# Kernel tuning notes

Measured on AMD Instinct MI355X. Metric: run time of the kernel, lower is better.

## Reference

```python
import jax, jax.numpy as jnp
import numpy as np

ACOUSTIC_BOOKS = [1, 2, 3, 4, 5, 6, 7, 8, 9, 10, 11, 12, 13, 14, 15, 16, 17, 17, 17, 17, 17]


def setup_inputs() -> dict:
    key = jax.random.key(0)
    ks = jax.random.split(key, 6)
    B, C, T, D, K, NB = 4, 512, 4096, 256, 2048, 18
    return {
        "x": jax.random.normal(ks[0], (B, C, T), dtype=jnp.float32),
        "Win_s": jax.random.normal(ks[1], (D, C), dtype=jnp.float32) * 0.05,
        "Win_a": jax.random.normal(ks[2], (D, C), dtype=jnp.float32) * 0.05,
        "Wout_s": jax.random.normal(ks[3], (C, D), dtype=jnp.float32) * 0.05,
        "Wout_a": jax.random.normal(ks[4], (C, D), dtype=jnp.float32) * 0.05,
        "E": jax.random.normal(ks[5], (NB, K, D), dtype=jnp.float32),
    }


def _nearest(z, e):
    # z: [B, D, T], e: [K, D] -> codes [B, T] via argmin of squared euclidean dist
    zt = z.transpose(0, 2, 1)  # [B, T, D]
    d2 = (jnp.sum(zt * zt, axis=-1, keepdims=True)
          - 2.0 * jnp.einsum('btd,kd->btk', zt, e)
          + jnp.sum(e * e, axis=-1))  # [B, T, K]
    return jnp.argmin(d2, axis=-1)  # [B, T]


def reference(x, Win_s, Win_a, Wout_s, Wout_a, E):
    # ---- encode ----
    xs = jnp.einsum('dc,bct->bdt', Win_s, x)  # in_proj_s (1x1 conv, no bias)
    codes = [_nearest(xs, E[0])]
    xa = jnp.einsum('dc,bct->bdt', Win_a, x)  # in_proj_a
    for cb in ACOUSTIC_BOOKS:
        idx = _nearest(xa, E[cb])
        xa = xa - E[cb][idx].transpose(0, 2, 1)  # residual subtract (decode gather)
        codes.append(idx)
    codes = jnp.stack(codes, axis=1)  # [B, 22, T]

    # ---- decode ----
    semantic = E[0][codes[:, 0]].transpose(0, 2, 1)  # [B, D, T]
    acoustic = jnp.zeros_like(semantic)
    for i, cb in enumerate(ACOUSTIC_BOOKS):
        acoustic = acoustic + E[cb][codes[:, i + 1]].transpose(0, 2, 1)
    out = (jnp.einsum('cd,bdt->bct', Wout_s, semantic)
           + jnp.einsum('cd,bdt->bct', Wout_a, acoustic))  # [B, 512, T]
    return out, codes
```

## Files before the change

### kernel.cpp

```cpp
#include <hip/hip_runtime.h>
#include <float.h>

#define TT 4096
#define BB 4
#define CC 512
#define DD 256
#define KK 2048
#define MM (BB*TT)
#define NBOOKS 22
#define EPS_PAIR 0.3f
#define EPS_FULL 0.3f
#define ZSTR 260
#define RPB 32

typedef _Float16 half8_t __attribute__((ext_vector_type(8)));
typedef float f32x4 __attribute__((ext_vector_type(4)));

__device__ __forceinline__ void insert3(float& v1, int& i1, float& v2, int& i2,
                                        float& v3, float u, int c) {
  if (u < v1 || (u == v1 && c < i1)) {
    v3 = v2; v2 = v1; i2 = i1; v1 = u; i1 = c;
  } else if (u < v2 || (u == v2 && c < i2)) {
    v3 = v2; v2 = u; i2 = c;
  } else {
    v3 = fminf(v3, u);
  }
}

__device__ __forceinline__ void merge5(float& v1, int& i1, float& v2, int& i2,
                                       float& v3,
                                       float w1, int j1, float w2, int j2, float w3) {
  if (w1 < v1 || (w1 == v1 && j1 < i1)) {
    if (v1 < w2 || (v1 == w2 && i1 < j2)) {
      v3 = fminf(v2, w2);
      v2 = v1; i2 = i1;
    } else {
      v3 = fminf(v1, w3);
      v2 = w2; i2 = j2;
    }
    v1 = w1; i1 = j1;
  } else {
    if (w1 < v2 || (w1 == v2 && j1 < i2)) {
      v3 = fminf(v2, w2);
      v2 = w1; i2 = j1;
    } else {
      v3 = fminf(w1, v3);
    }
  }
}

__global__ __launch_bounds__(256) void proj_kernel(const float* __restrict__ x,
    const float* __restrict__ Ws, const float* __restrict__ Wa,
    float* __restrict__ xs, float* __restrict__ xa)
{
  __shared__ float xt[16*64];
  __shared__ float wsl[16*68];
  __shared__ float wal[16*68];
  const int tid = threadIdx.x;
  const int t0 = blockIdx.x*64, d0 = blockIdx.y*64, b = blockIdx.z;
  const int u = tid & 63, cq = tid >> 6;
  const int tx = tid & 15, ty = tid >> 4;
  const float* xb = x + (size_t)b*CC*TT;
  float accS[4][4] = {{0}}, accA[4][4] = {{0}};
  for (int c0 = 0; c0 < CC; c0 += 16) {
    __syncthreads();
    #pragma unroll
    for (int i = 0; i < 4; ++i) {
      int cc = cq*4 + i;
      xt[cc*64 + u] = xb[(size_t)(c0+cc)*TT + t0 + u];
    }
    {
      float4 wv = *(const float4*)&Ws[(size_t)(d0+u)*CC + c0 + cq*4];
      wsl[(cq*4+0)*68 + u] = wv.x; wsl[(cq*4+1)*68 + u] = wv.y;
      wsl[(cq*4+2)*68 + u] = wv.z; wsl[(cq*4+3)*68 + u] = wv.w;
      wv = *(const float4*)&Wa[(size_t)(d0+u)*CC + c0 + cq*4];
      wal[(cq*4+0)*68 + u] = wv.x; wal[(cq*4+1)*68 + u] = wv.y;
      wal[(cq*4+2)*68 + u] = wv.z; wal[(cq*4+3)*68 + u] = wv.w;
    }
    __syncthreads();
    #pragma unroll
    for (int cc = 0; cc < 16; ++cc) {
      float4 tq = *(const float4*)&xt[cc*64 + ty*4];
      float4 sq = *(const float4*)&wsl[cc*68 + tx*4];
      float4 aq = *(const float4*)&wal[cc*68 + tx*4];
      float tf[4] = {tq.x,tq.y,tq.z,tq.w};
      float sf[4] = {sq.x,sq.y,sq.z,sq.w};
      float af[4] = {aq.x,aq.y,aq.z,aq.w};
      #pragma unroll
      for (int i = 0; i < 4; ++i)
        #pragma unroll
        for (int j = 0; j < 4; ++j) {
          accS[i][j] = fmaf(tf[i], sf[j], accS[i][j]);
          accA[i][j] = fmaf(tf[i], af[j], accA[i][j]);
        }
    }
  }
  #pragma unroll
  for (int i = 0; i < 4; ++i) {
    size_t r = (size_t)b*TT + t0 + ty*4 + i;
    float4 o;
    o.x = accS[i][0]; o.y = accS[i][1]; o.z = accS[i][2]; o.w = accS[i][3];
    *(float4*)&xs[r*DD + d0 + tx*4] = o;
    o.x = accA[i][0]; o.y = accA[i][1]; o.z = accA[i][2]; o.w = accA[i][3];
    *(float4*)&xa[r*DD + d0 + tx*4] = o;
  }
}

__global__ __launch_bounds__(256) void e2_kernel(const float* __restrict__ E,
    float* __restrict__ e2)
{
  int gid = blockIdx.x*256 + threadIdx.x;
  int wid = gid >> 6, lane = gid & 63;
  if (wid < 18*KK) {
    float4 v = *(const float4*)&E[(size_t)wid*DD + lane*4];
    float s = v.x*v.x + v.y*v.y + v.z*v.z + v.w*v.w;
    #pragma unroll
    for (int m = 1; m <= 32; m <<= 1) s += __shfl_xor(s, m);
    if (lane == 0) e2[wid] = s;
  }
}

__global__ __launch_bounds__(256) void cvt_e16_kernel(const float* __restrict__ E,
    _Float16* __restrict__ E16)
{
  size_t i = ((size_t)blockIdx.x*256 + threadIdx.x)*8;
  float4 u = *(const float4*)&E[i];
  float4 v = *(const float4*)&E[i+4];
  half8_t h;
  h[0]=(_Float16)u.x; h[1]=(_Float16)u.y; h[2]=(_Float16)u.z; h[3]=(_Float16)u.w;
  h[4]=(_Float16)v.x; h[5]=(_Float16)v.y; h[6]=(_Float16)v.z; h[7]=(_Float16)v.w;
  *(half8_t*)&E16[i] = h;
}

__global__ __launch_bounds__(256) __attribute__((amdgpu_waves_per_eu(2)))
void fused_encode_kernel(
    const float* __restrict__ xs_g, const float* __restrict__ xa_g,
    const float* __restrict__ E, const _Float16* __restrict__ E16,
    const float* __restrict__ e2, int* __restrict__ codes0,
    float* __restrict__ codes_f, float* __restrict__ aco_g)
{
  const int tid = threadIdx.x;
  const int lane = tid & 63, wave = tid >> 6;
  const int ln15 = lane & 15, lq = lane >> 4;
  const int row0 = blockIdx.x * RPB;

  __shared__ float Z[RPB][ZSTR];
  __shared__ float L1v[4][RPB], L2v[4][RPB], L3v[4][RPB];
  __shared__ int   L1i[4][RPB], L2i[4][RPB];
  __shared__ int   codes_s[RPB];
  __shared__ int   flist[RPB], plist[RPB];
  __shared__ int   nfull, npair;
  __shared__ float zrow[DD];
  __shared__ double Rv[4];
  __shared__ int    Ri[4];

  const int ldr = tid & 31, cg = tid >> 5;
  const int sr = tid >> 3, sg = tid & 7;

  for (int ib = 0; ib < NBOOKS; ++ib) {
    const int book = (ib <= 17) ? ib : 17;
    const float*     Eb   = E   + (size_t)book*KK*DD;
    const _Float16*  E16b = E16 + (size_t)book*KK*DD;
    const float*     e2b  = e2  + (size_t)book*KK;

    if (ib <= 1) {
      const float* src = (ib == 0) ? xs_g : xa_g;
      const float* sp = src + (size_t)(row0 + ldr)*DD + cg*32;
      #pragma unroll
      for (int j = 0; j < 8; ++j)
        *(float4*)&Z[ldr][cg*32 + j*4] = *(const float4*)(sp + j*4);
    }
    if (tid == 0) { nfull = 0; npair = 0; }
    __syncthreads();

    half8_t A[2][8];
    #pragma unroll
    for (int mt = 0; mt < 2; ++mt) {
      #pragma unroll
      for (int ks = 0; ks < 8; ++ks) {
        const float* zp = &Z[mt*16 + ln15][lq*8 + ks*32];
        float4 u = *(const float4*)zp;
        float4 v = *(const float4*)(zp + 4);
        half8_t a;
        a[0]=(_Float16)u.x; a[1]=(_Float16)u.y; a[2]=(_Float16)u.z; a[3]=(_Float16)u.w;
        a[4]=(_Float16)v.x; a[5]=(_Float16)v.y; a[6]=(_Float16)v.z; a[7]=(_Float16)v.w;
        A[mt][ks] = a;
      }
    }

    float b1[2][4], b2[2][4], b3[2][4]; int i1[2][4], i2[2][4];
    #pragma unroll
    for (int mt = 0; mt < 2; ++mt)
      #pragma unroll
      for (int j = 0; j < 4; ++j) {
        b1[mt][j] = FLT_MAX; b2[mt][j] = FLT_MAX; b3[mt][j] = FLT_MAX;
        i1[mt][j] = 0x7fffffff; i2[mt][j] = 0x7fffffff;
      }

    const _Float16* ebase = E16b + (size_t)(wave*512 + ln15)*DD + lq*8;

    half8_t B[8], NB[4];
    #pragma unroll
    for (int ks = 0; ks < 8; ++ks) B[ks] = *(const half8_t*)(ebase + ks*32);

    for (int nt = 0; nt < 32; ++nt) {
      const _Float16* nx = ebase + (size_t)(nt+1)*16*DD;
      if (nt < 31) {
        NB[0] = *(const half8_t*)(nx + 0*32);
        NB[1] = *(const half8_t*)(nx + 1*32);
        NB[2] = *(const half8_t*)(nx + 2*32);
        NB[3] = *(const half8_t*)(nx + 3*32);
      }
      int code = wave*512 + nt*16 + ln15;
      float e2v = e2b[code];
      f32x4 acc[2];
      #pragma unroll
      for (int mt = 0; mt < 2; ++mt) acc[mt] = (f32x4){0.f,0.f,0.f,0.f};
      #pragma unroll
      for (int ks = 0; ks < 8; ++ks) {
        #pragma unroll
        for (int mt = 0; mt < 2; ++mt)
          acc[mt] = __builtin_amdgcn_mfma_f32_16x16x32_f16(A[mt][ks], B[ks], acc[mt], 0, 0, 0);
      }
      #pragma unroll
      for (int mt = 0; mt < 2; ++mt)
        #pragma unroll
        for (int j = 0; j < 4; ++j) {
          float u = fmaf(-2.f, acc[mt][j], e2v);
          insert3(b1[mt][j], i1[mt][j], b2[mt][j], i2[mt][j], b3[mt][j], u, code);
        }
      if (nt < 31) {
        B[0] = NB[0]; B[1] = NB[1]; B[2] = NB[2]; B[3] = NB[3];
        B[4] = *(const half8_t*)(nx + 4*32);
        B[5] = *(const half8_t*)(nx + 5*32);
        B[6] = *(const half8_t*)(nx + 6*32);
        B[7] = *(const half8_t*)(nx + 7*32);
      }
    }

    #pragma unroll
    for (int mt = 0; mt < 2; ++mt)
      #pragma unroll
      for (int j = 0; j < 4; ++j) {
        float v1 = b1[mt][j], v2 = b2[mt][j], v3 = b3[mt][j];
        int a1 = i1[mt][j], a2 = i2[mt][j];
        #pragma unroll
        for (int m = 1; m <= 8; m <<= 1) {
          float w1 = __shfl_xor(v1, m), w2 = __shfl_xor(v2, m), w3 = __shfl_xor(v3, m);
          int   j1 = __shfl_xor(a1, m), j2 = __shfl_xor(a2, m);
          merge5(v1, a1, v2, a2, v3, w1, j1, w2, j2, w3);
        }
        if (ln15 == 0) {
          int rl = mt*16 + lq*4 + j;
          L1v[wave][rl] = v1; L1i[wave][rl] = a1;
          L2v[wave][rl] = v2; L2i[wave][rl] = a2;
          L3v[wave][rl] = v3;
        }
      }
    __syncthreads();
    if (tid < RPB) {
      float v1 = L1v[0][tid], v2 = L2v[0][tid], v3 = L3v[0][tid];
      int a1 = L1i[0][tid], a2 = L2i[0][tid];
      #pragma unroll
      for (int w = 1; w < 4; ++w)
        merge5(v1, a1, v2, a2, v3,
               L1v[w][tid], L1i[w][tid], L2v[w][tid], L2i[w][tid], L3v[w][tid]);
      codes_s[tid] = a1;
      int rg = row0 + tid;
      codes_f[((size_t)(rg >> 12)*NBOOKS + ib)*TT + (rg & (TT-1))] = (float)a1;
      if (ib == 0) codes0[rg] = a1;
      if (v3 - v1 < EPS_FULL) {
        flist[atomicAdd(&nfull, 1)] = tid;
      } else if (v2 - v1 < EPS_PAIR) {
        plist[atomicAdd(&npair, 1)] = tid | (a1 << 6) | (a2 << 17);
      }
    }
    __syncthreads();

    int nfl = nfull;
    for (int f = 0; f < nfl; ++f) {
      int row = flist[f];
      if (tid < 64)
        *(float4*)&zrow[tid*4] = *(const float4*)&Z[row][tid*4];
      __syncthreads();
      double bestv = DBL_MAX; int besti = 0x7fffffff;
      #pragma unroll
      for (int q = 0; q < 8; ++q) {
        int k = q*256 + tid;
        const float* er = Eb + (size_t)k*DD;
        double s = 0.0;
        for (int d = 0; d < DD; d += 4) {
          float4 e = *(const float4*)(er + d);
          double d0 = (double)zrow[d+0] - (double)e.x; s += d0*d0;
          double d1 = (double)zrow[d+1] - (double)e.y; s += d1*d1;
          double d2 = (double)zrow[d+2] - (double)e.z; s += d2*d2;
          double d3 = (double)zrow[d+3] - (double)e.w; s += d3*d3;
        }
        if (s < bestv || (s == bestv && k < besti)) { bestv = s; besti = k; }
      }
      #pragma unroll
      for (int m = 1; m <= 32; m <<= 1) {
        double ov = __shfl_xor(bestv, m);
        int    oi = __shfl_xor(besti, m);
        if (ov < bestv || (ov == bestv && oi < besti)) { bestv = ov; besti = oi; }
      }
      if (lane == 0) { Rv[wave] = bestv; Ri[wave] = besti; }
      __syncthreads();
      if (tid == 0) {
        double bvv = Rv[0]; int bii = Ri[0];
        #pragma unroll
        for (int w = 1; w < 4; ++w)
          if (Rv[w] < bvv || (Rv[w] == bvv && Ri[w] < bii)) { bvv = Rv[w]; bii = Ri[w]; }
        codes_s[row] = bii;
        int rg = row0 + row;
        codes_f[((size_t)(rg >> 12)*NBOOKS + ib)*TT + (rg & (TT-1))] = (float)bii;
        if (ib == 0) codes0[rg] = bii;
      }
      __syncthreads();
    }

    {
      int npr = npair;
      for (int f = wave; f < npr; f += 4) {
        int pk = plist[f];
        int row = pk & 63;
        int c1 = (pk >> 6) & 2047, c2 = (pk >> 17) & 2047;
        int cc = (lane < 32) ? c1 : c2;
        const float* er = Eb + (size_t)cc*DD + (lane & 31)*8;
        const float* zr = &Z[row][(lane & 31)*8];
        double s = 0.0;
        #pragma unroll
        for (int d = 0; d < 8; ++d) {
          double df = (double)zr[d] - (double)er[d];
          s += df*df;
        }
        #pragma unroll
        for (int m = 1; m <= 16; m <<= 1) s += __shfl_xor(s, m);
        double so = __shfl_xor(s, 32);
        double d1 = (lane < 32) ? s : so;
        double d2 = (lane < 32) ? so : s;
        int win = (d2 < d1 || (d2 == d1 && c2 < c1)) ? c2 : c1;
        if (lane == 0) {
          codes_s[row] = win;
          int rg = row0 + row;
          codes_f[((size_t)(rg >> 12)*NBOOKS + ib)*TT + (rg & (TT-1))] = (float)win;
          if (ib == 0) codes0[rg] = win;
        }
      }
    }
    __syncthreads();

    if (ib >= 1) {
      int code = codes_s[sr];
      const float* er = Eb + (size_t)code*DD;
      #pragma unroll
      for (int j = 0; j < 8; ++j) {
        int c = sg*4 + j*32;
        float4 e = *(const float4*)(er + c);
        float4 z = *(const float4*)&Z[sr][c];
        z.x -= e.x; z.y -= e.y; z.z -= e.z; z.w -= e.w;
        *(float4*)&Z[sr][c] = z;
      }
    }
    __syncthreads();
  }

  {
    const float* xp = xa_g + (size_t)(row0 + ldr)*DD + cg*32;
    float*       ap = aco_g + (size_t)(row0 + ldr)*DD + cg*32;
    #pragma unroll
    for (int j = 0; j < 8; ++j) {
      float4 x0 = *(const float4*)(xp + j*4);
      float4 zf = *(const float4*)&Z[ldr][cg*32 + j*4];
      float4 o;
      o.x = x0.x - zf.x; o.y = x0.y - zf.y; o.z = x0.z - zf.z; o.w = x0.w - zf.w;
      *(float4*)(ap + j*4) = o;
    }
  }
}

__global__ __launch_bounds__(256) void final_kernel(
    const float* __restrict__ Wos, const float* __restrict__ Woa,
    const float* __restrict__ E0, const int* __restrict__ codes0,
    const float* __restrict__ aco, float* __restrict__ out)
{
  __shared__ float wsl[16*68], wal[16*68], sml[16*68], acl[16*68];
  const int tid = threadIdx.x;
  const int t0 = blockIdx.x*64, c0 = blockIdx.y*64, b = blockIdx.z;
  const int u = tid & 63, dq = tid >> 6;
  const int tx = tid & 15, ty = tid >> 4;
  int code = codes0[b*TT + t0 + u];
  const float* smr = E0 + (size_t)code*DD;
  const float* acr = aco + (size_t)(b*TT + t0 + u)*DD;
  const float* wsr = Wos + (size_t)(c0+u)*DD;
  const float* war = Woa + (size_t)(c0+u)*DD;
  float accS[4][4] = {{0}}, accA[4][4] = {{0}};
  for (int dc0 = 0; dc0 < DD; dc0 += 16) {
    __syncthreads();
    float4 v;
    v = *(const float4*)(wsr + dc0 + dq*4);
    wsl[(dq*4+0)*68+u]=v.x; wsl[(dq*4+1)*68+u]=v.y; wsl[(dq*4+2)*68+u]=v.z; wsl[(dq*4+3)*68+u]=v.w;
    v = *(const float4*)(war + dc0 + dq*4);
    wal[(dq*4+0)*68+u]=v.x; wal[(dq*4+1)*68+u]=v.y; wal[(dq*4+2)*68+u]=v.z; wal[(dq*4+3)*68+u]=v.w;
    v = *(const float4*)(smr + dc0 + dq*4);
    sml[(dq*4+0)*68+u]=v.x; sml[(dq*4+1)*68+u]=v.y; sml[(dq*4+2)*68+u]=v.z; sml[(dq*4+3)*68+u]=v.w;
    v = *(const float4*)(acr + dc0 + dq*4);
    acl[(dq*4+0)*68+u]=v.x; acl[(dq*4+1)*68+u]=v.y; acl[(dq*4+2)*68+u]=v.z; acl[(dq*4+3)*68+u]=v.w;
    __syncthreads();
    #pragma unroll
    for (int d = 0; d < 16; ++d) {
      float4 cs = *(const float4*)&wsl[d*68 + tx*4];
      float4 ca = *(const float4*)&wal[d*68 + tx*4];
      float4 ts = *(const float4*)&sml[d*68 + ty*4];
      float4 ta = *(const float4*)&acl[d*68 + ty*4];
      float csf[4]={cs.x,cs.y,cs.z,cs.w}, caf[4]={ca.x,ca.y,ca.z,ca.w};
      float tsf[4]={ts.x,ts.y,ts.z,ts.w}, taf[4]={ta.x,ta.y,ta.z,ta.w};
      #pragma unroll
      for (int i = 0; i < 4; ++i)
        #pragma unroll
        for (int j = 0; j < 4; ++j) {
          accS[i][j] = fmaf(csf[i], tsf[j], accS[i][j]);
          accA[i][j] = fmaf(caf[i], taf[j], accA[i][j]);
        }
    }
  }
  size_t ob = (size_t)b*CC*TT;
  #pragma unroll
  for (int i = 0; i < 4; ++i) {
    float4 r;
    r.x = accS[i][0] + accA[i][0];
    r.y = accS[i][1] + accA[i][1];
    r.z = accS[i][2] + accA[i][2];
    r.w = accS[i][3] + accA[i][3];
    *(float4*)&out[ob + (size_t)(c0 + tx*4 + i)*TT + t0 + ty*4] = r;
  }
}

extern "C" void kernel_launch(void* const* d_in, const int* in_sizes, int n_in,
                              void* d_out, int out_size, void* d_ws, size_t ws_size,
                              hipStream_t stream) {
  const float* x    = (const float*)d_in[0];
  const float* Wins = (const float*)d_in[1];
  const float* Wina = (const float*)d_in[2];
  const float* Wos  = (const float*)d_in[3];
  const float* Woa  = (const float*)d_in[4];
  const float* E    = (const float*)d_in[5];
  float* out = (float*)d_out;
  float* codes_f = out + (size_t)BB*CC*TT;

  _Float16* E16 = (_Float16*)d_out;

  float* xs  = (float*)d_ws;
  float* xa  = xs + (size_t)MM*DD;
  float* aco = xa + (size_t)MM*DD;
  float* e2  = aco + (size_t)MM*DD;
  int* codes_i = (int*)(e2 + 18*KK);

  proj_kernel<<<dim3(TT/64, DD/64, BB), 256, 0, stream>>>(x, Wins, Wina, xs, xa);
  e2_kernel<<<(18*KK*64)/256, 256, 0, stream>>>(E, e2);
  cvt_e16_kernel<<<(18*KK*DD)/8/256, 256, 0, stream>>>(E, E16);

  fused_encode_kernel<<<MM/RPB, 256, 0, stream>>>(xs, xa, E, E16, e2,
                                                  codes_i, codes_f, aco);

  final_kernel<<<dim3(TT/64, CC/64, BB), 256, 0, stream>>>(Wos, Woa, E, codes_i, aco, out);
}
```

Measured before the change: 1.881 ms.

## Pack score and code into sortable uint keys for top-3 tracking

```diff
diff --git a/kernel.cpp b/kernel.cpp
--- a/kernel.cpp
+++ b/kernel.cpp
@@ -8,45 +8,29 @@
 #define KK 2048
 #define MM (BB*TT)
 #define NBOOKS 22
-#define EPS_PAIR 0.3f
-#define EPS_FULL 0.3f
-#define ZSTR 260
+#define EPS_PAIR 0.5f
+#define EPS_FULL 0.5f
+#define ZSTR 352
 #define RPB 32
 
 typedef _Float16 half8_t __attribute__((ext_vector_type(8)));
 typedef float f32x4 __attribute__((ext_vector_type(4)));
 
-__device__ __forceinline__ void insert3(float& v1, int& i1, float& v2, int& i2,
-                                        float& v3, float u, int c) {
-  if (u < v1 || (u == v1 && c < i1)) {
-    v3 = v2; v2 = v1; i2 = i1; v1 = u; i1 = c;
-  } else if (u < v2 || (u == v2 && c < i2)) {
-    v3 = v2; v2 = u; i2 = c;
-  } else {
-    v3 = fminf(v3, u);
-  }
-}
-
-__device__ __forceinline__ void merge5(float& v1, int& i1, float& v2, int& i2,
-                                       float& v3,
-                                       float w1, int j1, float w2, int j2, float w3) {
-  if (w1 < v1 || (w1 == v1 && j1 < i1)) {
-    if (v1 < w2 || (v1 == w2 && i1 < j2)) {
-      v3 = fminf(v2, w2);
-      v2 = v1; i2 = i1;
-    } else {
-      v3 = fminf(v1, w3);
-      v2 = w2; i2 = j2;
-    }
-    v1 = w1; i1 = j1;
-  } else {
-    if (w1 < v2 || (w1 == v2 && j1 < i2)) {
-      v3 = fminf(v2, w2);
-      v2 = w1; i2 = j1;
-    } else {
-      v3 = fminf(w1, v3);
-    }
-  }
+__device__ __forceinline__ uint32_t packsc(float s, int code) {
+  uint32_t b = __float_as_uint(s);
+  uint32_t key = b ^ ((uint32_t)((int32_t)b >> 31) | 0x80000000u);
+  return (key & 0xFFFFF800u) | (uint32_t)code;
+}
+__device__ __forceinline__ float unpacksc(uint32_t p) {
+  uint32_t key = p & 0xFFFFF800u;
+  uint32_t b = (key & 0x80000000u) ? (key ^ 0x80000000u) : ~key;
+  return __uint_as_float(b);
+}
+__device__ __forceinline__ void ins3(uint32_t& v1, uint32_t& v2, uint32_t& v3,
+                                     uint32_t p) {
+  uint32_t t1 = max(v1, p); v1 = min(v1, p);
+  uint32_t t2 = max(v2, t1); v2 = min(v2, t1);
+  v3 = min(v3, t2);
 }
 
 __global__ __launch_bounds__(256) void proj_kernel(const float* __restrict__ x,
@@ -132,7 +116,7 @@
   *(half8_t*)&E16[i] = h;
 }
 
-__global__ __launch_bounds__(256) __attribute__((amdgpu_waves_per_eu(2)))
+__global__ __launch_bounds__(256) __attribute__((amdgpu_waves_per_eu(3,3)))
 void fused_encode_kernel(
     const float* __restrict__ xs_g, const float* __restrict__ xa_g,
     const float* __restrict__ E, const _Float16* __restrict__ E16,
@@ -145,12 +129,10 @@
   const int row0 = blockIdx.x * RPB;
 
   __shared__ float Z[RPB][ZSTR];
-  __shared__ float L1v[4][RPB], L2v[4][RPB], L3v[4][RPB];
-  __shared__ int   L1i[4][RPB], L2i[4][RPB];
+  __shared__ uint32_t L1[4][RPB], L2[4][RPB], L3[4][RPB];
   __shared__ int   codes_s[RPB];
   __shared__ int   flist[RPB], plist[RPB];
   __shared__ int   nfull, npair;
-  __shared__ float zrow[DD];
   __shared__ double Rv[4];
   __shared__ int    Ri[4];
 
@@ -188,29 +170,21 @@
       }
     }
 
-    float b1[2][4], b2[2][4], b3[2][4]; int i1[2][4], i2[2][4];
+    uint32_t p1[2][4], p2[2][4], p3[2][4];
     #pragma unroll
     for (int mt = 0; mt < 2; ++mt)
       #pragma unroll
       for (int j = 0; j < 4; ++j) {
-        b1[mt][j] = FLT_MAX; b2[mt][j] = FLT_MAX; b3[mt][j] = FLT_MAX;
-        i1[mt][j] = 0x7fffffff; i2[mt][j] = 0x7fffffff;
+        p1[mt][j] = 0xFFFFFFFFu; p2[mt][j] = 0xFFFFFFFFu; p3[mt][j] = 0xFFFFFFFFu;
       }
 
     const _Float16* ebase = E16b + (size_t)(wave*512 + ln15)*DD + lq*8;
 
-    half8_t B[8], NB[4];
-    #pragma unroll
-    for (int ks = 0; ks < 8; ++ks) B[ks] = *(const half8_t*)(ebase + ks*32);
-
     for (int nt = 0; nt < 32; ++nt) {
-      const _Float16* nx = ebase + (size_t)(nt+1)*16*DD;
-      if (nt < 31) {
-        NB[0] = *(const half8_t*)(nx + 0*32);
-        NB[1] = *(const half8_t*)(nx + 1*32);
-        NB[2] = *(const half8_t*)(nx + 2*32);
-        NB[3] = *(const half8_t*)(nx + 3*32);
-      }
+      const _Float16* bp = ebase + (size_t)nt*16*DD;
+      half8_t B[8];
+      #pragma unroll
+      for (int ks = 0; ks < 8; ++ks) B[ks] = *(const half8_t*)(bp + ks*32);
       int code = wave*512 + nt*16 + ln15;
       float e2v = e2b[code];
       f32x4 acc[2];
@@ -227,51 +201,47 @@
         #pragma unroll
         for (int j = 0; j < 4; ++j) {
           float u = fmaf(-2.f, acc[mt][j], e2v);
-          insert3(b1[mt][j], i1[mt][j], b2[mt][j], i2[mt][j], b3[mt][j], u, code);
-        }
-      if (nt < 31) {
-        B[0] = NB[0]; B[1] = NB[1]; B[2] = NB[2]; B[3] = NB[3];
-        B[4] = *(const half8_t*)(nx + 4*32);
-        B[5] = *(const half8_t*)(nx + 5*32);
-        B[6] = *(const half8_t*)(nx + 6*32);
-        B[7] = *(const half8_t*)(nx + 7*32);
-      }
+          ins3(p1[mt][j], p2[mt][j], p3[mt][j], packsc(u, code));
+        }
     }
 
     #pragma unroll
     for (int mt = 0; mt < 2; ++mt)
       #pragma unroll
       for (int j = 0; j < 4; ++j) {
-        float v1 = b1[mt][j], v2 = b2[mt][j], v3 = b3[mt][j];
-        int a1 = i1[mt][j], a2 = i2[mt][j];
+        uint32_t v1 = p1[mt][j], v2 = p2[mt][j], v3 = p3[mt][j];
         #pragma unroll
         for (int m = 1; m <= 8; m <<= 1) {
-          float w1 = __shfl_xor(v1, m), w2 = __shfl_xor(v2, m), w3 = __shfl_xor(v3, m);
-          int   j1 = __shfl_xor(a1, m), j2 = __shfl_xor(a2, m);
-          merge5(v1, a1, v2, a2, v3, w1, j1, w2, j2, w3);
+          uint32_t w1 = (uint32_t)__shfl_xor((int)v1, m);
+          uint32_t w2 = (uint32_t)__shfl_xor((int)v2, m);
+          uint32_t w3 = (uint32_t)__shfl_xor((int)v3, m);
+          ins3(v1, v2, v3, w1);
+          ins3(v1, v2, v3, w2);
+          ins3(v1, v2, v3, w3);
         }
         if (ln15 == 0) {
           int rl = mt*16 + lq*4 + j;
-          L1v[wave][rl] = v1; L1i[wave][rl] = a1;
-          L2v[wave][rl] = v2; L2i[wave][rl] = a2;
-          L3v[wave][rl] = v3;
+          L1[wave][rl] = v1; L2[wave][rl] = v2; L3[wave][rl] = v3;
         }
       }
     __syncthreads();
     if (tid < RPB) {
-      float v1 = L1v[0][tid], v2 = L2v[0][tid], v3 = L3v[0][tid];
-      int a1 = L1i[0][tid], a2 = L2i[0][tid];
-      #pragma unroll
-      for (int w = 1; w < 4; ++w)
-        merge5(v1, a1, v2, a2, v3,
-               L1v[w][tid], L1i[w][tid], L2v[w][tid], L2i[w][tid], L3v[w][tid]);
+      uint32_t v1 = L1[0][tid], v2 = L2[0][tid], v3 = L3[0][tid];
+      #pragma unroll
+      for (int w = 1; w < 4; ++w) {
+        ins3(v1, v2, v3, L1[w][tid]);
+        ins3(v1, v2, v3, L2[w][tid]);
+        ins3(v1, v2, v3, L3[w][tid]);
+      }
+      int a1 = (int)(v1 & 2047u), a2 = (int)(v2 & 2047u);
+      float f1 = unpacksc(v1), f2 = unpacksc(v2), f3 = unpacksc(v3);
       codes_s[tid] = a1;
       int rg = row0 + tid;
       codes_f[((size_t)(rg >> 12)*NBOOKS + ib)*TT + (rg & (TT-1))] = (float)a1;
       if (ib == 0) codes0[rg] = a1;
-      if (v3 - v1 < EPS_FULL) {
+      if (f3 - f1 < EPS_FULL) {
         flist[atomicAdd(&nfull, 1)] = tid;
-      } else if (v2 - v1 < EPS_PAIR) {
+      } else if (f2 - f1 < EPS_PAIR) {
         plist[atomicAdd(&npair, 1)] = tid | (a1 << 6) | (a2 << 17);
       }
     }
@@ -280,9 +250,6 @@
     int nfl = nfull;
     for (int f = 0; f < nfl; ++f) {
       int row = flist[f];
-      if (tid < 64)
-        *(float4*)&zrow[tid*4] = *(const float4*)&Z[row][tid*4];
-      __syncthreads();
       double bestv = DBL_MAX; int besti = 0x7fffffff;
       #pragma unroll
       for (int q = 0; q < 8; ++q) {
@@ -291,10 +258,10 @@
         double s = 0.0;
         for (int d = 0; d < DD; d += 4) {
           float4 e = *(const float4*)(er + d);
-          double d0 = (double)zrow[d+0] - (double)e.x; s += d0*d0;
-          double d1 = (double)zrow[d+1] - (double)e.y; s += d1*d1;
-          double d2 = (double)zrow[d+2] - (double)e.z; s += d2*d2;
-          double d3 = (double)zrow[d+3] - (double)e.w; s += d3*d3;
+          double d0 = (double)Z[row][d+0] - (double)e.x; s += d0*d0;
+          double d1 = (double)Z[row][d+1] - (double)e.y; s += d1*d1;
+          double d2 = (double)Z[row][d+2] - (double)e.z; s += d2*d2;
+          double d3 = (double)Z[row][d+3] - (double)e.w; s += d3*d3;
         }
         if (s < bestv || (s == bestv && k < besti)) { bestv = s; besti = k; }
       }
```

Result: slower. 1.953 ms (+3.9%).
